# Kernel optimization log

Measured on AMD Instinct MI355X. Metric: run time of the kernel, lower is better.

The kernel has to match this reference:

```python
import jax, jax.numpy as jnp
import numpy as np

B, NOBJ, QD, VD = 128, 36, 2400, 2048
N = B * NOBJ
NEG_SLOPE = 0.2


def _edges():
    # fully connected per image, self-loops included (PyG GATConv adds them)
    base = np.arange(NOBJ)
    src = np.repeat(base, NOBJ)
    dst = np.tile(base, NOBJ)
    off = (np.arange(B) * NOBJ)[:, None]
    return np.stack([(src[None] + off).reshape(-1), (dst[None] + off).reshape(-1)])


def setup_inputs() -> dict:
    key = jax.random.key(0)
    ks = jax.random.split(key, 24)
    p = lambda k, shape, fan: jax.random.normal(k, shape, jnp.float32) * (1.0 / np.sqrt(fan))
    inp = {
        "question_embedding": jax.random.normal(ks[0], (B, QD), jnp.float32),
        "object_features": jax.random.normal(ks[1], (N, VD), jnp.float32),
        "edge_index": jnp.asarray(_edges(), jnp.int32),
        "Wq": p(ks[2], (QD, 2048), QD), "bq": jnp.zeros((2048,), jnp.float32),
        "Wv": p(ks[3], (VD, 2048), VD), "bv": jnp.zeros((2048,), jnp.float32),
        "W1": p(ks[4], (2048, 4 * 256), 2048), "a1s": p(ks[5], (4, 256), 256),
        "a1d": p(ks[6], (4, 256), 256), "b1": jnp.zeros((1024,), jnp.float32),
        "W2": p(ks[7], (1024, 4 * 256), 1024), "a2s": p(ks[8], (4, 256), 256),
        "a2d": p(ks[9], (4, 256), 256), "b2": jnp.zeros((1024,), jnp.float32),
        "W3": p(ks[10], (1024, 5 * 512), 1024), "a3s": p(ks[11], (5, 512), 512),
        "a3d": p(ks[12], (5, 512), 512), "b3": jnp.zeros((512,), jnp.float32),
        "batch_size": B, "num_obj": NOBJ,
    }
    return inp


def gat_conv(x, edge_index, W, a_src, a_dst, b, heads, ch, concat):
    n = x.shape[0]
    h = (x @ W).reshape(n, heads, ch)                       # [N,H,C]
    src, dst = edge_index[0], edge_index[1]
    al_s = jnp.einsum('nhc,hc->nh', h, a_src)               # [N,H]
    al_d = jnp.einsum('nhc,hc->nh', h, a_dst)
    e = jax.nn.leaky_relu(al_s[src] + al_d[dst], NEG_SLOPE)  # [E,H]
    # segment softmax over edges sharing a destination node
    e_max = jax.ops.segment_max(e, dst, num_segments=n)
    e = jnp.exp(e - e_max[dst])
    denom = jax.ops.segment_sum(e, dst, num_segments=n)
    alpha = e / (denom[dst] + 1e-16)                        # [E,H]
    msg = h[src] * alpha[:, :, None]                        # [E,H,C]
    out = jax.ops.segment_sum(msg, dst, num_segments=n)     # [N,H,C]
    out = out.reshape(n, heads * ch) if concat else out.mean(axis=1)
    return out + b


def reference(question_embedding, object_features, edge_index,
              Wq, bq, Wv, bv,
              W1, a1s, a1d, b1,
              W2, a2s, a2d, b2,
              W3, a3s, a3d, b3,
              batch_size, num_obj):
    # hadamard fusion of question with per-object features
    q = question_embedding @ Wq + bq                        # [B,2048]
    q = jnp.repeat(q, num_obj, axis=0)                      # [N,2048]
    v = object_features @ Wv + bv
    x = q * v
    g1 = jax.nn.relu(gat_conv(x, edge_index, W1, a1s, a1d, b1, 4, 256, True))
    g2 = jax.nn.relu(gat_conv(g1, edge_index, W2, a2s, a2d, b2, 4, 256, True))
    g2 = g2 + g1                                            # residual
    return gat_conv(g2, edge_index, W3, a3s, a3d, b3, 5, 512, False)
```

## Files before the change

### kernel.cpp

```cpp
#include <hip/hip_runtime.h>
#include <hip/hip_bf16.h>

typedef unsigned short u16;
typedef __bf16 bf16x8 __attribute__((ext_vector_type(8)));
typedef float f32x4 __attribute__((ext_vector_type(4)));

#define B_IMG 128
#define NOBJ  36
#define NNODE (B_IMG * NOBJ)

__device__ __forceinline__ float b2f(u16 u) {
    union { unsigned int i; float f; } v; v.i = ((unsigned int)u) << 16; return v.f;
}
__device__ __forceinline__ u16 f2b(float f) {
    union { float f; unsigned int i; } v; v.f = f;
    unsigned int u = v.i;
    return (u16)((u + 0x7fffu + ((u >> 16) & 1u)) >> 16);
}

__global__ __launch_bounds__(256)
void conv_all(const float* __restrict__ of, u16* __restrict__ of_c,
              const float* __restrict__ qe, u16* __restrict__ qe_c)
{
    const int bid = blockIdx.x;
    if (bid < 9216) {
        const int i = bid * 256 + threadIdx.x;
        const float4 f = ((const float4*)of)[i];
        ushort4 o; o.x = f2b(f.x); o.y = f2b(f.y); o.z = f2b(f.z); o.w = f2b(f.w);
        ((ushort4*)of_c)[i] = o;
    } else {
        const int i = (bid - 9216) * 256 + threadIdx.x;
        const int r = i / 2560, c = i - r * 2560;
        qe_c[i] = (c < 2400) ? f2b(qe[r * 2400 + c]) : (u16)0;
    }
}

__global__ __launch_bounds__(256)
void transpose_cvt2(const float* __restrict__ s0, u16* __restrict__ d0,
                    int Rs0, int Rd0, int C0, int nt0,
                    const float* __restrict__ s1, u16* __restrict__ d1,
                    int Rs1, int Rd1, int C1)
{
    __shared__ u16 tile[32][33];
    int tb = blockIdx.x;
    const float* src; u16* dst; int Rs, Rd, C;
    if (tb < nt0) { src = s0; dst = d0; Rs = Rs0; Rd = Rd0; C = C0; }
    else { tb -= nt0; src = s1; dst = d1; Rs = Rs1; Rd = Rd1; C = C1; }
    const int ntx = C >> 5;
    const int ty = tb / ntx, tx = tb - ty * ntx;
    const int bx = tx * 32, by = ty * 32;
    const int lx = threadIdx.x & 31, ly = threadIdx.x >> 5;
    #pragma unroll
    for (int i = ly; i < 32; i += 8) {
        const int k = by + i;
        tile[i][lx] = (k < Rs) ? f2b(src[(size_t)k * C + bx + lx]) : (u16)0;
    }
    __syncthreads();
    #pragma unroll
    for (int i = ly; i < 32; i += 8) dst[(size_t)(bx + i) * Rd + by + lx] = tile[lx][i];
}

template<int EPI>
__global__ __launch_bounds__(256, 3)
void gemm_tn(const u16* __restrict__ A, const u16* __restrict__ Bt,
             int M, int N, int K, int kLen,
             float* __restrict__ Cf, u16* __restrict__ Cb,
             const float* __restrict__ bias, const float* __restrict__ qmul)
{
    __shared__ __align__(16) u16 lds[3 * 8192];

    const int t    = threadIdx.x;
    const int lane = t & 63;
    const int wave = t >> 6;
    const int wr = wave >> 1, wc = wave & 1;
    const int quad = lane >> 4, l16 = lane & 15;
    const int rowBase = blockIdx.y * 128;
    const int colBase = blockIdx.x * 128;
    const int k0 = blockIdx.z * kLen;

    const int lq = (lane & 3) ^ ((lane >> 3) & 3);
    const u16* gA0 = A  + (size_t)(rowBase + wave * 32 + (lane >> 2)) * K + k0 + lq * 8;
    const u16* gA1 = gA0 + 16 * (size_t)K;
    const u16* gB0 = Bt + (size_t)(colBase + wave * 32 + (lane >> 2)) * K + k0 + lq * 8;
    const u16* gB1 = gB0 + 16 * (size_t)K;
    const int ro = wave * 1024;

    const int sw = (quad ^ ((l16 >> 1) & 3)) * 8;
    int afr[4], bfr[4];
    #pragma unroll
    for (int r = 0; r < 4; r++) afr[r] = (wr * 64 + r * 16 + l16) * 32 + sw;
    #pragma unroll
    for (int c = 0; c < 4; c++) bfr[c] = 4096 + (wc * 64 + c * 16 + l16) * 32 + sw;

    f32x4 acc[4][4];
    #pragma unroll
    for (int r = 0; r < 4; r++)
        #pragma unroll
        for (int c = 0; c < 4; c++)
            acc[r][c] = (f32x4){0.f, 0.f, 0.f, 0.f};

    auto gld = [](const u16* g, u16* s) {
        __builtin_amdgcn_global_load_lds(
            (const __attribute__((address_space(1))) void*)g,
            (__attribute__((address_space(3))) void*)s, 16, 0, 0);
    };
    auto dma_stage = [&](int it, int st) {
        const int kk = it * 32;
        const int bo = st * 8192;
        gld(gA0 + kk, &lds[bo + ro]);
        gld(gA1 + kk, &lds[bo + ro + 512]);
        gld(gB0 + kk, &lds[bo + 4096 + ro]);
        gld(gB1 + kk, &lds[bo + 4096 + ro + 512]);
    };

    const int nIter = kLen >> 5;
    dma_stage(0, 0);
    dma_stage(1, 1);
    int st = 0, st2 = 2;
    for (int it = 0; it < nIter; ++it) {
        if (it + 1 < nIter) asm volatile("s_waitcnt vmcnt(4)\n\ts_barrier" ::: "memory");
        else                asm volatile("s_waitcnt vmcnt(0)\n\ts_barrier" ::: "memory");
        if (it + 2 < nIter) dma_stage(it + 2, st2);
        const int bo = st * 8192;
        bf16x8 avf[4], bvf[4];
        #pragma unroll
        for (int r = 0; r < 4; r++) avf[r] = *(const bf16x8*)&lds[bo + afr[r]];
        #pragma unroll
        for (int c = 0; c < 4; c++) bvf[c] = *(const bf16x8*)&lds[bo + bfr[c]];
        #pragma unroll
        for (int r = 0; r < 4; r++)
            #pragma unroll
            for (int c = 0; c < 4; c++)
                acc[r][c] = __builtin_amdgcn_mfma_f32_16x16x32_bf16(avf[r], bvf[c], acc[r][c], 0, 0, 0);
        st  = (st  == 2) ? 0 : st  + 1;
        st2 = (st2 == 2) ? 0 : st2 + 1;
    }

    #pragma unroll
    for (int r = 0; r < 4; r++) {
        const int mBase = rowBase + wr * 64 + r * 16 + quad * 4;
        #pragma unroll
        for (int c = 0; c < 4; c++) {
            const int n = colBase + wc * 64 + c * 16 + l16;
            #pragma unroll
            for (int e = 0; e < 4; e++) {
                const int m = mBase + e;
                float v = acc[r][c][e];
                if (EPI == 1) {
                    Cf[((size_t)blockIdx.z * M + m) * N + n] = v;
                } else if (EPI == 2) {
                    v += bias[n];
                    v *= qmul[(size_t)(m / NOBJ) * N + n];
                    Cb[(size_t)m * N + n] = f2b(v);
                } else {
                    Cb[(size_t)m * N + n] = f2b(v);
                }
            }
        }
    }
}

__global__ __launch_bounds__(256)
void qcombine(const float* __restrict__ p, const float* __restrict__ bias,
              float* __restrict__ q, int MN, int S)
{
    const int i = blockIdx.x * 256 + threadIdx.x;
    float s = 0.f;
    for (int z = 0; z < S; z++) s += p[(size_t)z * MN + i];
    q[i] = s + bias[i & 2047];
}

template<int H, int C, bool MEAN>
__global__ __launch_bounds__(256)
void al_alpha(const u16* __restrict__ h, const float* __restrict__ a_s,
              const float* __restrict__ a_d, float* __restrict__ alphaG)
{
    __shared__ float asl[36], adl[36];
    const int hd = blockIdx.x, b = blockIdx.y;
    const int nb = b * NOBJ;
    const int t = threadIdx.x, wv = t >> 6, lane = t & 63;
    constexpr int PL = C / 64;
    const float* asp = a_s + hd * C + lane * PL;
    const float* adp = a_d + hd * C + lane * PL;
    for (int n = wv; n < 36; n += 4) {
        const u16* hp = h + (size_t)(nb + n) * (H * C) + hd * C + lane * PL;
        u16 hb[PL];
        if constexpr (PL == 4) { *(uint2*)hb = *(const uint2*)hp; }
        else                   { *(uint4*)hb = *(const uint4*)hp; }
        float s1 = 0.f, s2 = 0.f;
        #pragma unroll
        for (int i = 0; i < PL; i++) {
            const float hv = b2f(hb[i]);
            s1 += hv * asp[i];
            s2 += hv * adp[i];
        }
        #pragma unroll
        for (int off = 32; off > 0; off >>= 1) {
            s1 += __shfl_down(s1, off);
            s2 += __shfl_down(s2, off);
        }
        if (lane == 0) { asl[n] = s1; adl[n] = s2; }
    }
    __syncthreads();
    if (t >= 36) return;
    const float ad = adl[t];
    float row[36];
    float mx = -1e30f;
    #pragma unroll
    for (int s = 0; s < 36; s++) {
        float v = asl[s] + ad; v = (v > 0.f) ? v : 0.2f * v;
        row[s] = v; mx = fmaxf(mx, v);
    }
    float sum = 0.f;
    #pragma unroll
    for (int s = 0; s < 36; s++) { row[s] = expf(row[s] - mx); sum += row[s]; }
    const float inv = (MEAN ? 0.2f : 1.0f) / (sum + 1e-16f);
    float* o = alphaG + (((size_t)b * H + hd) * 36 + t) * 36;
    #pragma unroll
    for (int s = 0; s < 36; s++) o[s] = row[s] * inv;
}

template<int H, int C, int MODE>
__global__ __launch_bounds__(192)
void attn_agg(const u16* __restrict__ h, const float* __restrict__ alphaG,
              const float* __restrict__ bias, const u16* __restrict__ resid,
              u16* __restrict__ outb)
{
    constexpr int NSLAB = C / 64;
    __shared__ __align__(16) u16 hl[36 * 64];
    __shared__ float al[36 * 36];
    const int b = blockIdx.y;
    const int hd = blockIdx.x / NSLAB, sl = blockIdx.x - hd * NSLAB;
    const int nb = b * NOBJ, cb = sl * 64;
    const int t = threadIdx.x;

    for (int e = t; e < 36 * 8; e += 192) {
        const int row = e >> 3, col = (e & 7) * 8;
        *(uint4*)&hl[row * 64 + col] =
            *(const uint4*)&h[(size_t)(nb + row) * (H * C) + hd * C + cb + col];
    }
    const float* ap = alphaG + ((size_t)b * H + hd) * 1296;
    for (int e = t; e < 1296; e += 192) al[e] = ap[e];
    __syncthreads();

    #pragma unroll
    for (int p = 0; p < 3; p++) {
        const int e = p * 192 + t;
        const int d = e >> 4, c4 = (e & 15) * 4;
        float a0 = 0, a1 = 0, a2 = 0, a3 = 0;
        for (int s = 0; s < 36; s++) {
            const float av = al[d * 36 + s];
            const ushort4 hv = *(const ushort4*)&hl[s * 64 + c4];
            a0 += av * b2f(hv.x); a1 += av * b2f(hv.y);
            a2 += av * b2f(hv.z); a3 += av * b2f(hv.w);
        }
        const int n = nb + d;
        const size_t base = (size_t)n * (H * C) + hd * C + cb + c4;
        const int bb = hd * C + cb + c4;
        float v0 = a0 + bias[bb + 0];
        float v1 = a1 + bias[bb + 1];
        float v2 = a2 + bias[bb + 2];
        float v3 = a3 + bias[bb + 3];
        v0 = v0 > 0.f ? v0 : 0.f; v1 = v1 > 0.f ? v1 : 0.f;
        v2 = v2 > 0.f ? v2 : 0.f; v3 = v3 > 0.f ? v3 : 0.f;
        if (MODE == 2) {
            v0 += b2f(resid[base + 0]); v1 += b2f(resid[base + 1]);
            v2 += b2f(resid[base + 2]); v3 += b2f(resid[base + 3]);
        }
        outb[base + 0] = f2b(v0); outb[base + 1] = f2b(v1);
        outb[base + 2] = f2b(v2); outb[base + 3] = f2b(v3);
    }
}

__global__ __launch_bounds__(192)
void attn_agg_mean(const u16* __restrict__ h, const float* __restrict__ alphaG,
                   const float* __restrict__ b3, float* __restrict__ outp)
{
    __shared__ __align__(16) u16 hl[36 * 64];
    __shared__ float al[36 * 36];
    const int b = blockIdx.y, sl = blockIdx.x;
    const int nb = b * NOBJ, cb = sl * 64;
    const int t = threadIdx.x;

    float acc[3][4] = {};
    for (int hd = 0; hd < 5; hd++) {
        if (hd) __syncthreads();
        for (int e = t; e < 36 * 8; e += 192) {
            const int row = e >> 3, col = (e & 7) * 8;
            *(uint4*)&hl[row * 64 + col] =
                *(const uint4*)&h[(size_t)(nb + row) * 2560 + hd * 512 + cb + col];
        }
        const float* ap = alphaG + ((size_t)b * 5 + hd) * 1296;
        for (int e = t; e < 1296; e += 192) al[e] = ap[e];
        __syncthreads();
        #pragma unroll
        for (int p = 0; p < 3; p++) {
            const int e = p * 192 + t;
            const int d = e >> 4, c4 = (e & 15) * 4;
            for (int s = 0; s < 36; s++) {
                const float av = al[d * 36 + s];
                const ushort4 hv = *(const ushort4*)&hl[s * 64 + c4];
                acc[p][0] += av * b2f(hv.x); acc[p][1] += av * b2f(hv.y);
                acc[p][2] += av * b2f(hv.z); acc[p][3] += av * b2f(hv.w);
            }
        }
    }
    #pragma unroll
    for (int p = 0; p < 3; p++) {
        const int e = p * 192 + t;
        const int d = e >> 4, c4 = (e & 15) * 4;
        #pragma unroll
        for (int j = 0; j < 4; j++)
            outp[(size_t)(nb + d) * 512 + cb + c4 + j] = acc[p][j] + b3[cb + c4 + j];
    }
}

extern "C" void kernel_launch(void* const* d_in, const int* in_sizes, int n_in,
                              void* d_out, int out_size, void* d_ws, size_t ws_size,
                              hipStream_t stream)
{
    const float* qe  = (const float*)d_in[0];
    const float* of  = (const float*)d_in[1];
    const float* Wq  = (const float*)d_in[3];
    const float* bq  = (const float*)d_in[4];
    const float* Wv  = (const float*)d_in[5];
    const float* bv  = (const float*)d_in[6];
    const float* W1  = (const float*)d_in[7];
    const float* a1s = (const float*)d_in[8];
    const float* a1d = (const float*)d_in[9];
    const float* b1  = (const float*)d_in[10];
    const float* W2  = (const float*)d_in[11];
    const float* a2s = (const float*)d_in[12];
    const float* a2d = (const float*)d_in[13];
    const float* b2  = (const float*)d_in[14];
    const float* W3  = (const float*)d_in[15];
    const float* a3s = (const float*)d_in[16];
    const float* a3d = (const float*)d_in[17];
    const float* b3  = (const float*)d_in[18];
    float* out = (float*)d_out;
    (void)ws_size; (void)in_sizes; (void)n_in; (void)out_size;

    char* W0 = (char*)d_ws;
    size_t off = 0;
    auto alloc = [&](size_t bytes) -> char* {
        char* p = W0 + off; off += (bytes + 255) & ~(size_t)255; return p;
    };
    u16* qe_c = (u16*)alloc(128ull * 2560 * 2);
    u16* of_c = (u16*)alloc(4608ull * 2048 * 2);
    const size_t szA = 4608ull * 2560 * 2;
    const size_t szB = 4608ull * 1024 * 2;
    const size_t szC = 4608ull * 1024 * 2;
    char* Abase = alloc(szA);
    char* Bbase = alloc(szB);
    char* Cbase = alloc(szC);
    float* alphaG = (float*)alloc(128ull * 5 * 36 * 36 * 4);

    u16*   WqT   = (u16*)Abase;
    float* qpart = (float*)(Abase + 2048ull * 2560 * 2);
    u16*   x     = (u16*)Abase;
    u16*   g1    = (u16*)Abase;
    u16*   h3    = (u16*)Abase;
    u16*   WvT   = (u16*)Bbase;
    float* q     = (float*)(Bbase + 2048ull * 2048 * 2);
    u16*   W1T   = (u16*)Bbase;
    u16*   W2T   = (u16*)(Bbase + 1024ull * 2048 * 2);
    u16*   g2    = (u16*)Bbase;
    u16*   h1    = (u16*)Cbase;
    u16*   h2    = (u16*)Cbase;
    u16*   W3T   = (u16*)Cbase;

    conv_all<<<dim3(9216 + 1280), 256, 0, stream>>>(of, of_c, qe, qe_c);

    transpose_cvt2<<<dim3(5120 + 4096), 256, 0, stream>>>(
        Wq, WqT, 2400, 2560, 2048, 5120,
        Wv, WvT, 2048, 2048, 2048);

    gemm_tn<1><<<dim3(16, 1, 5), 256, 0, stream>>>(qe_c, WqT, 128, 2048, 2560, 512,
                                                   qpart, nullptr, nullptr, nullptr);
    qcombine<<<dim3(128 * 2048 / 256), 256, 0, stream>>>(qpart, bq, q, 128 * 2048, 5);

    gemm_tn<2><<<dim3(16, 36, 1), 256, 0, stream>>>(of_c, WvT, 4608, 2048, 2048, 2048,
                                                    nullptr, x, bv, q);

    transpose_cvt2<<<dim3(2048 + 1024), 256, 0, stream>>>(
        W1, W1T, 2048, 2048, 1024, 2048,
        W2, W2T, 1024, 1024, 1024);

    gemm_tn<0><<<dim3(8, 36, 1), 256, 0, stream>>>(x, W1T, 4608, 1024, 2048, 2048,
                                                   nullptr, h1, nullptr, nullptr);
    al_alpha<4, 256, false><<<dim3(4, B_IMG), 256, 0, stream>>>(h1, a1s, a1d, alphaG);
    attn_agg<4, 256, 1><<<dim3(16, B_IMG), 192, 0, stream>>>(h1, alphaG, b1, nullptr, g1);

    gemm_tn<0><<<dim3(8, 36, 1), 256, 0, stream>>>(g1, W2T, 4608, 1024, 1024, 1024,
                                                   nullptr, h2, nullptr, nullptr);
    al_alpha<4, 256, false><<<dim3(4, B_IMG), 256, 0, stream>>>(h2, a2s, a2d, alphaG);
    attn_agg<4, 256, 2><<<dim3(16, B_IMG), 192, 0, stream>>>(h2, alphaG, b2, g1, g2);

    transpose_cvt2<<<dim3(2560), 256, 0, stream>>>(
        W3, W3T, 1024, 1024, 2560, 2560,
        W3, W3T, 1024, 1024, 2560);
    gemm_tn<0><<<dim3(20, 36, 1), 256, 0, stream>>>(g2, W3T, 4608, 2560, 1024, 1024,
                                                    nullptr, h3, nullptr, nullptr);
    al_alpha<5, 512, true><<<dim3(5, B_IMG), 256, 0, stream>>>(h3, a3s, a3d, alphaG);
    attn_agg_mean<<<dim3(8, B_IMG), 192, 0, stream>>>(h3, alphaG, b3, out);
}
```

Baseline: 478.6 us.

## Load GEMM A operand directly to registers and fuse GAT attention kernels

The GEMM now loads the A operand from global memory straight into registers and stages only B through LDS. This halves LDS use per block, moves to double buffering and raises the occupancy hint from 3 to 4 blocks. Separately, the per-layer alpha computation and aggregation for layers 1 and 2 are fused into one kernel per head and image, which drops the global alpha buffer round trip and one launch per layer. The risks are uncoalesced A loads, a full vmcnt(0) wait each step that limits latency hiding, and fewer, larger attention blocks (512 instead of 2048).

```diff
diff --git a/kernel.cpp b/kernel.cpp
--- a/kernel.cpp
+++ b/kernel.cpp
@@ -61,13 +61,13 @@
 }
 
 template<int EPI>
-__global__ __launch_bounds__(256, 3)
+__global__ __launch_bounds__(256, 4)
 void gemm_tn(const u16* __restrict__ A, const u16* __restrict__ Bt,
              int M, int N, int K, int kLen,
              float* __restrict__ Cf, u16* __restrict__ Cb,
              const float* __restrict__ bias, const float* __restrict__ qmul)
 {
-    __shared__ __align__(16) u16 lds[3 * 8192];
+    __shared__ __align__(16) u16 lds[2 * 4096];
 
     const int t    = threadIdx.x;
     const int lane = t & 63;
@@ -78,19 +78,16 @@
     const int colBase = blockIdx.x * 128;
     const int k0 = blockIdx.z * kLen;
 
-    const int lq = (lane & 3) ^ ((lane >> 3) & 3);
-    const u16* gA0 = A  + (size_t)(rowBase + wave * 32 + (lane >> 2)) * K + k0 + lq * 8;
-    const u16* gA1 = gA0 + 16 * (size_t)K;
-    const u16* gB0 = Bt + (size_t)(colBase + wave * 32 + (lane >> 2)) * K + k0 + lq * 8;
+    const u16* gB0 = Bt + (size_t)(colBase + wave * 32 + (lane >> 2)) * K + k0 + (lane & 3) * 8;
     const u16* gB1 = gB0 + 16 * (size_t)K;
     const int ro = wave * 1024;
 
-    const int sw = (quad ^ ((l16 >> 1) & 3)) * 8;
-    int afr[4], bfr[4];
-    #pragma unroll
-    for (int r = 0; r < 4; r++) afr[r] = (wr * 64 + r * 16 + l16) * 32 + sw;
-    #pragma unroll
-    for (int c = 0; c < 4; c++) bfr[c] = 4096 + (wc * 64 + c * 16 + l16) * 32 + sw;
+    const u16* gA = A + (size_t)(rowBase + wr * 64 + l16) * K + k0 + quad * 8;
+    const size_t aRow16 = (size_t)16 * K;
+
+    int bfr[4];
+    #pragma unroll
+    for (int c = 0; c < 4; c++) bfr[c] = (wc * 64 + c * 16 + l16) * 32 + quad * 8;
 
     f32x4 acc[4][4];
     #pragma unroll
@@ -104,36 +101,40 @@
             (const __attribute__((address_space(1))) void*)g,
             (__attribute__((address_space(3))) void*)s, 16, 0, 0);
     };
-    auto dma_stage = [&](int it, int st) {
+    auto dmaB = [&](int it, int st) {
         const int kk = it * 32;
-        const int bo = st * 8192;
-        gld(gA0 + kk, &lds[bo + ro]);
-        gld(gA1 + kk, &lds[bo + ro + 512]);
-        gld(gB0 + kk, &lds[bo + 4096 + ro]);
-        gld(gB1 + kk, &lds[bo + 4096 + ro + 512]);
+        const int bo = st * 4096;
+        gld(gB0 + kk, &lds[bo + ro]);
+        gld(gB1 + kk, &lds[bo + ro + 512]);
     };
-
-    const int nIter = kLen >> 5;
-    dma_stage(0, 0);
-    dma_stage(1, 1);
-    int st = 0, st2 = 2;
-    for (int it = 0; it < nIter; ++it) {
-        if (it + 1 < nIter) asm volatile("s_waitcnt vmcnt(4)\n\ts_barrier" ::: "memory");
-        else                asm volatile("s_waitcnt vmcnt(0)\n\ts_barrier" ::: "memory");
-        if (it + 2 < nIter) dma_stage(it + 2, st2);
-        const int bo = st * 8192;
-        bf16x8 avf[4], bvf[4];
-        #pragma unroll
-        for (int r = 0; r < 4; r++) avf[r] = *(const bf16x8*)&lds[bo + afr[r]];
-        #pragma unroll
-        for (int c = 0; c < 4; c++) bvf[c] = *(const bf16x8*)&lds[bo + bfr[c]];
+    auto loadA = [&](bf16x8* d, int it) {
+        const u16* p = gA + it * 32;
+        #pragma unroll
+        for (int r = 0; r < 4; r++) d[r] = *(const bf16x8*)(p + (size_t)r * aRow16);
+    };
+    auto compute = [&](int st, const bf16x8* av) {
+        const int bo = st * 4096;
+        bf16x8 bv[4];
+        #pragma unroll
+        for (int c = 0; c < 4; c++) bv[c] = *(const bf16x8*)&lds[bo + bfr[c]];
         #pragma unroll
         for (int r = 0; r < 4; r++)
             #pragma unroll
             for (int c = 0; c < 4; c++)
-                acc[r][c] = __builtin_amdgcn_mfma_f32_16x16x32_bf16(avf[r], bvf[c], acc[r][c], 0, 0, 0);
-        st  = (st  == 2) ? 0 : st  + 1;
-        st2 = (st2 == 2) ? 0 : st2 + 1;
+                acc[r][c] = __builtin_amdgcn_mfma_f32_16x16x32_bf16(av[r], bv[c], acc[r][c], 0, 0, 0);
+    };
+
+    const int nIter = kLen >> 5;
+    bf16x8 a0[4], a1[4];
+    dmaB(0, 0);
+    loadA(a0, 0);
+    for (int it = 0; it < nIter; it += 2) {
+        asm volatile("s_waitcnt vmcnt(0)\n\ts_barrier" ::: "memory");
+        if (it + 1 < nIter) { dmaB(it + 1, 1); loadA(a1, it + 1); }
+        compute(0, a0);
+        asm volatile("s_waitcnt vmcnt(0)\n\ts_barrier" ::: "memory");
+        if (it + 2 < nIter) { dmaB(it + 2, 0); loadA(a0, it + 2); }
+        compute(1, a1);
     }
 
     #pragma unroll
@@ -170,6 +171,87 @@
     q[i] = s + bias[i & 2047];
 }
 
+template<int H, int C, int MODE>
+__global__ __launch_bounds__(256)
+void attn_kernel(const u16* __restrict__ h, const float* __restrict__ a_src,
+                 const float* __restrict__ a_dst, const float* __restrict__ bias,
+                 const u16* __restrict__ resid, u16* __restrict__ outb)
+{
+    __shared__ __align__(16) u16 hl[36 * C];
+    __shared__ float alpha[36 * 36];
+    __shared__ float asl[36], adl[36];
+    __shared__ float psum[36][8][2];
+    const int b = blockIdx.y, hd = blockIdx.x;
+    const int t = threadIdx.x;
+    const int nb = b * NOBJ;
+    constexpr int CH = C / 8;
+    for (int e = t; e < 36 * CH; e += 256) {
+        const int row = e / CH, col = (e - row * CH) * 8;
+        *(uint4*)&hl[row * C + col] = *(const uint4*)&h[(size_t)(nb + row) * (H * C) + hd * C + col];
+    }
+    __syncthreads();
+    constexpr int SEG = C / 8;
+    for (int e = t; e < 36 * 8; e += 256) {
+        const int n = e >> 3, sg = e & 7;
+        const u16*   hp = &hl[n * C + sg * SEG];
+        const float* as = a_src + hd * C + sg * SEG;
+        const float* ad = a_dst + hd * C + sg * SEG;
+        float s1 = 0.f, s2 = 0.f;
+        #pragma unroll 8
+        for (int i = 0; i < SEG; i++) {
+            const float hv = b2f(hp[i]);
+            s1 += hv * as[i]; s2 += hv * ad[i];
+        }
+        psum[n][sg][0] = s1; psum[n][sg][1] = s2;
+    }
+    __syncthreads();
+    if (t < 36) {
+        float s1 = 0.f, s2 = 0.f;
+        #pragma unroll
+        for (int sg = 0; sg < 8; sg++) { s1 += psum[t][sg][0]; s2 += psum[t][sg][1]; }
+        asl[t] = s1; adl[t] = s2;
+    }
+    __syncthreads();
+    if (t < 36) {
+        const float ad = adl[t];
+        float mx = -1e30f;
+        for (int s = 0; s < 36; s++) {
+            float v = asl[s] + ad; v = (v > 0.f) ? v : 0.2f * v;
+            alpha[t * 36 + s] = v; mx = fmaxf(mx, v);
+        }
+        float sum = 0.f;
+        for (int s = 0; s < 36; s++) { const float ex = expf(alpha[t * 36 + s] - mx); alpha[t * 36 + s] = ex; sum += ex; }
+        const float inv = 1.f / (sum + 1e-16f);
+        for (int s = 0; s < 36; s++) alpha[t * 36 + s] *= inv;
+    }
+    __syncthreads();
+    constexpr int NC4 = C / 4;
+    for (int e = t; e < 36 * NC4; e += 256) {
+        const int d = e / NC4, c4 = (e - d * NC4) * 4;
+        float a0 = 0, a1 = 0, a2 = 0, a3 = 0;
+        for (int s = 0; s < 36; s++) {
+            const float al = alpha[d * 36 + s];
+            const ushort4 hv = *(const ushort4*)&hl[s * C + c4];
+            a0 += al * b2f(hv.x); a1 += al * b2f(hv.y); a2 += al * b2f(hv.z); a3 += al * b2f(hv.w);
+        }
+        const int n = nb + d;
+        const size_t base = (size_t)n * (H * C) + hd * C + c4;
+        const int bb = hd * C + c4;
+        float v0 = a0 + bias[bb + 0];
+        float v1 = a1 + bias[bb + 1];
+        float v2 = a2 + bias[bb + 2];
+        float v3 = a3 + bias[bb + 3];
+        v0 = v0 > 0.f ? v0 : 0.f; v1 = v1 > 0.f ? v1 : 0.f;
+        v2 = v2 > 0.f ? v2 : 0.f; v3 = v3 > 0.f ? v3 : 0.f;
+        if (MODE == 2) {
+            v0 += b2f(resid[base + 0]); v1 += b2f(resid[base + 1]);
+            v2 += b2f(resid[base + 2]); v3 += b2f(resid[base + 3]);
+        }
+        outb[base + 0] = f2b(v0); outb[base + 1] = f2b(v1);
+        outb[base + 2] = f2b(v2); outb[base + 3] = f2b(v3);
+    }
+}
+
 template<int H, int C, bool MEAN>
 __global__ __launch_bounds__(256)
 void al_alpha(const u16* __restrict__ h, const float* __restrict__ a_s,
@@ -218,58 +300,6 @@
     float* o = alphaG + (((size_t)b * H + hd) * 36 + t) * 36;
     #pragma unroll
     for (int s = 0; s < 36; s++) o[s] = row[s] * inv;
-}
-
-template<int H, int C, int MODE>
-__global__ __launch_bounds__(192)
-void attn_agg(const u16* __restrict__ h, const float* __restrict__ alphaG,
-              const float* __restrict__ bias, const u16* __restrict__ resid,
-              u16* __restrict__ outb)
-{
-    constexpr int NSLAB = C / 64;
-    __shared__ __align__(16) u16 hl[36 * 64];
-    __shared__ float al[36 * 36];
-    const int b = blockIdx.y;
-    const int hd = blockIdx.x / NSLAB, sl = blockIdx.x - hd * NSLAB;
-    const int nb = b * NOBJ, cb = sl * 64;
-    const int t = threadIdx.x;
-
-    for (int e = t; e < 36 * 8; e += 192) {
-        const int row = e >> 3, col = (e & 7) * 8;
-        *(uint4*)&hl[row * 64 + col] =
-            *(const uint4*)&h[(size_t)(nb + row) * (H * C) + hd * C + cb + col];
-    }
-    const float* ap = alphaG + ((size_t)b * H + hd) * 1296;
-    for (int e = t; e < 1296; e += 192) al[e] = ap[e];
-    __syncthreads();
-
-    #pragma unroll
-    for (int p = 0; p < 3; p++) {
-        const int e = p * 192 + t;
-        const int d = e >> 4, c4 = (e & 15) * 4;
-        float a0 = 0, a1 = 0, a2 = 0, a3 = 0;
-        for (int s = 0; s < 36; s++) {
-            const float av = al[d * 36 + s];
-            const ushort4 hv = *(const ushort4*)&hl[s * 64 + c4];
-            a0 += av * b2f(hv.x); a1 += av * b2f(hv.y);
-            a2 += av * b2f(hv.z); a3 += av * b2f(hv.w);
-        }
-        const int n = nb + d;
-        const size_t base = (size_t)n * (H * C) + hd * C + cb + c4;
-        const int bb = hd * C + cb + c4;
-        float v0 = a0 + bias[bb + 0];
-        float v1 = a1 + bias[bb + 1];
-        float v2 = a2 + bias[bb + 2];
-        float v3 = a3 + bias[bb + 3];
-        v0 = v0 > 0.f ? v0 : 0.f; v1 = v1 > 0.f ? v1 : 0.f;
-        v2 = v2 > 0.f ? v2 : 0.f; v3 = v3 > 0.f ? v3 : 0.f;
-        if (MODE == 2) {
-            v0 += b2f(resid[base + 0]); v1 += b2f(resid[base + 1]);
-            v2 += b2f(resid[base + 2]); v3 += b2f(resid[base + 3]);
-        }
-        outb[base + 0] = f2b(v0); outb[base + 1] = f2b(v1);
-        outb[base + 2] = f2b(v2); outb[base + 3] = f2b(v3);
-    }
 }
 
 __global__ __launch_bounds__(192)
@@ -388,13 +418,11 @@
 
     gemm_tn<0><<<dim3(8, 36, 1), 256, 0, stream>>>(x, W1T, 4608, 1024, 2048, 2048,
                                                    nullptr, h1, nullptr, nullptr);
-    al_alpha<4, 256, false><<<dim3(4, B_IMG), 256, 0, stream>>>(h1, a1s, a1d, alphaG);
-    attn_agg<4, 256, 1><<<dim3(16, B_IMG), 192, 0, stream>>>(h1, alphaG, b1, nullptr, g1);
+    attn_kernel<4, 256, 1><<<dim3(4, B_IMG), 256, 0, stream>>>(h1, a1s, a1d, b1, nullptr, g1);
 
     gemm_tn<0><<<dim3(8, 36, 1), 256, 0, stream>>>(g1, W2T, 4608, 1024, 1024, 1024,
                                                    nullptr, h2, nullptr, nullptr);
-    al_alpha<4, 256, false><<<dim3(4, B_IMG), 256, 0, stream>>>(h2, a2s, a2d, alphaG);
-    attn_agg<4, 256, 2><<<dim3(16, B_IMG), 192, 0, stream>>>(h2, alphaG, b2, g1, g2);
+    attn_kernel<4, 256, 2><<<dim3(4, B_IMG), 256, 0, stream>>>(h2, a2s, a2d, b2, g1, g2);
 
     transpose_cvt2<<<dim3(2560), 256, 0, stream>>>(
         W3, W3T, 1024, 1024, 2560, 2560,
```

New measurement: 804.1 us. 1.68x slower.
